# Kernel tuning notes

Hardware: AMD Instinct MI355X
Metric: run time of the kernel (lower is better)

## Reference

```python
import jax, jax.numpy as jnp
import numpy as np

HEADS, DIM_HEAD = 4, 32
EAF_LAMBDA, EAF_ZMAX = 1.0, 4.0
MIN_SIGMA, MAX_SIGMA = 1.0, 8.0

def _gen_grid(h, w):
    xs = np.linspace(0.0, 1.0, w, dtype=np.float32)
    ys = np.linspace(0.0, 1.0, h, dtype=np.float32)
    gy, gx = np.meshgrid(ys, xs, indexing='ij')
    return np.stack([gx, gy, np.ones_like(gx)], 0)  # [3,h,w]

def setup_inputs():
    key = jax.random.key(0)
    ks = jax.random.split(key, 12)
    B, N, C, D = 4, 6, 128, 128
    Hb, Wb, fh, fw = 25, 25, 24, 48
    inner = HEADS * DIM_HEAD
    # BEV ego-plane grid (same math as BEVEmbedding with bev 200x200, 100m, 3 decoder blocks)
    g = _gen_grid(Hb, Wb)
    g[0] *= 200.0
    g[1] *= 200.0
    V = np.array([[0., -2., 100.], [-2., 0., 100.], [0., 0., 1.]], dtype=np.float32)
    bev_grid = (np.linalg.inv(V) @ g.reshape(3, -1)).reshape(3, Hb, Wb)
    # image plane pixel grid (buffer), scaled to 480x224 image
    ip = _gen_grid(fh, fw)[None]
    ip[:, 0] *= 480.0
    ip[:, 1] *= 224.0
    # cam->world extrinsics: 6 surround cameras on a ring
    E_inv = np.zeros((B, N, 4, 4), dtype=np.float32)
    for n in range(N):
        yaw = 2.0 * np.pi * n / N
        c, s = np.cos(yaw), np.sin(yaw)
        E_inv[:, n, :3, :3] = np.array([[c, -s, 0.], [s, c, 0.], [0., 0., 1.]], dtype=np.float32)
        E_inv[:, n, :3, 3] = np.array([2. * c, 2. * s, 1.6], dtype=np.float32)
        E_inv[:, n, 3, 3] = 1.0
    Kmat = np.array([[260., 0., 240.], [0., 260., 112.], [0., 0., 1.]], dtype=np.float32)
    I_inv = np.broadcast_to(np.linalg.inv(Kmat), (B, N, 3, 3)).astype(np.float32).copy()
    w = lambda k, shape: 0.02 * jax.random.normal(k, shape, dtype=jnp.float32)
    return dict(
        x=jax.random.normal(ks[0], (B, D, Hb, Wb), dtype=jnp.float32),
        feature=jax.random.normal(ks[1], (B, N, C, fh, fw), dtype=jnp.float32),
        I_inv=jnp.asarray(I_inv), E_inv=jnp.asarray(E_inv),
        bev_grid=jnp.asarray(bev_grid), image_plane=jnp.asarray(ip),
        bn_v_g=jnp.ones(C), bn_v_b=jnp.zeros(C), bn_v_m=jnp.zeros(C), bn_v_var=jnp.ones(C),
        conv_v_w=w(ks[2], (D, C)),
        bn_k_g=jnp.ones(C), bn_k_b=jnp.zeros(C), bn_k_m=jnp.zeros(C), bn_k_var=jnp.ones(C),
        conv_k_w=w(ks[3], (D, C)),
        ln_q_g=jnp.ones(D), ln_q_b=jnp.zeros(D),
        ln_k_g=jnp.ones(D), ln_k_b=jnp.zeros(D),
        ln_v_g=jnp.ones(D), ln_v_b=jnp.zeros(D),
        Wq=w(ks[4], (inner, D)), bq=jnp.zeros(inner),
        Wk=w(ks[5], (inner, D)), bk=jnp.zeros(inner),
        Wv=w(ks[6], (inner, D)), bv=jnp.zeros(inner),
        Wo=w(ks[7], (D, inner)), bo=jnp.zeros(D),
        ln_pre_g=jnp.ones(D), ln_pre_b=jnp.zeros(D),
        W1=w(ks[8], (2 * D, D)), b1=jnp.zeros(2 * D),
        W2=w(ks[9], (D, 2 * D)), b2=jnp.zeros(D),
        ln_post_g=jnp.ones(D), ln_post_b=jnp.zeros(D),
    )

def _ln(x, g, b):
    m = x.mean(-1, keepdims=True)
    v = ((x - m) ** 2).mean(-1, keepdims=True)
    return (x - m) * jax.lax.rsqrt(v + 1e-5) * g + b

def _bn_relu_conv(f, g, b, mu, var, Wc):
    # inference BatchNorm2d -> ReLU -> 1x1 Conv (no bias)
    f = (f - mu[None, :, None, None]) * (jax.lax.rsqrt(var + 1e-5) * g)[None, :, None, None] + b[None, :, None, None]
    f = jax.nn.relu(f)
    return jnp.einsum('bchw,dc->bdhw', f, Wc)

def reference(x, feature, I_inv, E_inv, bev_grid, image_plane,
              bn_v_g, bn_v_b, bn_v_m, bn_v_var, conv_v_w,
              bn_k_g, bn_k_b, bn_k_m, bn_k_var, conv_k_w,
              ln_q_g, ln_q_b, ln_k_g, ln_k_b, ln_v_g, ln_v_b,
              Wq, bq, Wk, bk, Wv, bv, Wo, bo,
              ln_pre_g, ln_pre_b, W1, b1, W2, b2, ln_post_g, ln_post_b):
    B, N, C, fh, fw = feature.shape
    _, D, Hb, Wb = x.shape
    Q = Hb * Wb
    Kp = fh * fw
    feat = feature.reshape(B * N, C, fh, fw)
    val = _bn_relu_conv(feat, bn_v_g, bn_v_b, bn_v_m, bn_v_var, conv_v_w)
    keyf = _bn_relu_conv(feat, bn_k_g, bn_k_b, bn_k_m, bn_k_var, conv_k_w)
    v = val.reshape(B, N, D, fh, fw)
    k = keyf.reshape(B, N, D, fh, fw)
    # ---- EAF weights ----
    xy = bev_grid[:2].reshape(2, Q).T                      # [Q,2]
    ones = jnp.ones((Q, 1), dtype=bev_grid.dtype)
    P0 = jnp.concatenate([xy, 0.0 * ones, ones], -1)       # [Q,4] z=0
    P1 = jnp.concatenate([xy, EAF_ZMAX * ones, ones], -1)  # [Q,4] z=zmax
    E = jnp.linalg.inv(E_inv)                              # world->cam
    P0c = jnp.einsum('bnij,qj->bnqi', E, P0)
    P1c = jnp.einsum('bnij,qj->bnqi', E, P1)
    Icam = jnp.linalg.inv(I_inv)
    p0 = jnp.einsum('bnij,bnqj->bnqi', Icam, P0c[..., :3])
    p1 = jnp.einsum('bnij,bnqj->bnqi', Icam, P1c[..., :3])
    p0 = p0 / (p0[..., 2:3] + 1e-8)
    p1 = p1 / (p1[..., 2:3] + 1e-8)
    l = jnp.cross(p0, p1)                                  # epipolar line [B,N,Q,3]
    denom = jnp.maximum(jnp.sqrt(l[..., 0] ** 2 + l[..., 1] ** 2), 1e-8)
    l_hat = l / denom[..., None]
    x_img = image_plane[0].reshape(3, Kp).T                # [K,3]
    d = jnp.abs(jnp.einsum('bnqj,kj->bnqk', l_hat, x_img))
    # adaptive lambda_{q,i}
    cam_xy = E_inv[..., :2, 3]                             # [B,N,2]
    vec = xy[None, None] - cam_xy[:, :, None]              # [B,N,Q,2]
    dist = jnp.linalg.norm(vec, axis=-1) + 1e-6
    dist_max = dist.max(axis=(1, 2), keepdims=True) + 1e-6
    dist_norm = jnp.clip(dist / dist_max, 0.0, 1.0)
    sigma = MAX_SIGMA - dist_norm * (MAX_SIGMA - MIN_SIGMA)
    lambda_qi = 1.0 / (sigma + 1e-6)
    scale_w = (EAF_LAMBDA * lambda_qi) ** 2                # [B,N,Q]
    Wmask = jnp.exp(-scale_w[..., None] * d ** 2)          # [B,N,Q,K]
    W_logits = Wmask.transpose(0, 2, 1, 3).reshape(B, Q, N * Kp)
    # ---- cross attention (EAF weight multiplied into logits pre-softmax) ----
    qt = x.reshape(B, D, Q).transpose(0, 2, 1)             # [B,Q,D]
    kt = k.transpose(0, 1, 3, 4, 2).reshape(B, N * Kp, D)
    vt = v.transpose(0, 1, 3, 4, 2).reshape(B, N * Kp, D)
    qp = _ln(qt, ln_q_g, ln_q_b) @ Wq.T + bq
    kp = _ln(kt, ln_k_g, ln_k_b) @ Wk.T + bk
    vp = _ln(vt, ln_v_g, ln_v_b) @ Wv.T + bv
    qh = qp.reshape(B, Q, HEADS, DIM_HEAD).transpose(0, 2, 1, 3)
    kh = kp.reshape(B, N * Kp, HEADS, DIM_HEAD).transpose(0, 2, 1, 3)
    vh = vp.reshape(B, N * Kp, HEADS, DIM_HEAD).transpose(0, 2, 1, 3)
    logits = jnp.einsum('bhqd,bhkd->bhqk', qh, kh) * (DIM_HEAD ** -0.5)
    logits = logits * W_logits[:, None]                    # broadcast over heads
    attn = jax.nn.softmax(logits, axis=-1)
    out = jnp.einsum('bhqk,bhkd->bhqd', attn, vh)
    out = out.transpose(0, 2, 1, 3).reshape(B, Q, HEADS * DIM_HEAD)
    out = out @ Wo.T + bo                                  # [B,Q,D]
    z = out + qt                                           # skip = x
    z = _ln(z, ln_pre_g, ln_pre_b)
    z = z + (jax.nn.gelu(z @ W1.T + b1, approximate=False) @ W2.T + b2)
    z = _ln(z, ln_post_g, ln_post_b)
    return z.transpose(0, 2, 1).reshape(B, D, Hb, Wb)
```

## Files before the change

### kernel.cpp

```cpp
#include <hip/hip_runtime.h>
#include <hip/hip_bf16.h>

typedef unsigned short u16;
typedef __attribute__((ext_vector_type(8))) short short8v;
typedef __attribute__((ext_vector_type(4))) float f32x4;
typedef __attribute__((ext_vector_type(2))) __fp16 fp16x2;

#define B_   4
#define N_   6
#define Q_   625
#define QPAD 640
#define KP_  1152
#define NK_  6912
#define NKB  216
#define NSPLIT 12
#define KSEG (NK_/NSPLIT)
#define FHW  1152
#define LOG2E 1.4426950408889634f
#define LOG2_LOG2E 0.5287663729448977f

__device__ __forceinline__ float bfu(unsigned int u16v){ return __uint_as_float(u16v << 16); }
__device__ __forceinline__ unsigned int f2bfu(float f){
  unsigned int u = __float_as_uint(f);
  return (u + 0x7fffu + ((u>>16)&1u)) >> 16;
}
__device__ __forceinline__ float exp2a(float x){
  float r; asm("v_exp_f32 %0, %1" : "=v"(r) : "v"(x)); return r;
}
__device__ __forceinline__ unsigned cvtpk_bf16(float lo, float hi){
  unsigned r; asm("v_cvt_pk_bf16_f32 %0, %1, %2" : "=v"(r) : "v"(lo), "v"(hi)); return r;
}
__device__ __forceinline__ unsigned cvtpk_f16(float lo, float hi){
  union { fp16x2 h; unsigned u; } c;
  c.h = __builtin_amdgcn_cvt_pkrtz(lo, hi);
  return c.u;
}
__device__ __forceinline__ float ldfeat(const void* p, size_t i, bool isbf){
  return isbf ? bfu((unsigned)reinterpret_cast<const u16*>(p)[i])
              : reinterpret_cast<const float*>(p)[i];
}
union U4S8 { uint4 u; short8v s; };
union H2U { unsigned u; fp16x2 h; };

struct InPack {
  const void* p[38];
  int off[38];
  int sz[38];
  int nseg;
  int total;
};

__global__ __launch_bounds__(256) void k_ingest(InPack P, float* __restrict__ dst,
                                                const unsigned* __restrict__ magic){
  int idx = blockIdx.x*256 + threadIdx.x;
  if (idx >= P.total) return;
  bool isbf = (*magic == 0x3F803F80u);
  int lo=0, hi=P.nseg-1;
  while (lo<hi){ int mid=(lo+hi+1)>>1; if (P.off[mid]<=idx) lo=mid; else hi=mid-1; }
  int j = idx - P.off[lo];
  float v = 0.f;
  if (j < P.sz[lo]){
    v = isbf ? bfu((unsigned)reinterpret_cast<const u16*>(P.p[lo])[j])
             : reinterpret_cast<const float*>(P.p[lo])[j];
  }
  dst[idx] = v;
}

__global__ void k_prep(const float* __restrict__ ckw, const float* __restrict__ cvw,
                       const float* __restrict__ Wk,  const float* __restrict__ Wv,
                       const float* __restrict__ Wq,  const float* __restrict__ Wo,
                       const float* __restrict__ W1,  const float* __restrict__ W2,
                       const float* __restrict__ bkg, const float* __restrict__ bkb,
                       const float* __restrict__ bkm, const float* __restrict__ bkv,
                       const float* __restrict__ bvg, const float* __restrict__ bvb,
                       const float* __restrict__ bvm, const float* __restrict__ bvv,
                       u16* convKbf, u16* convVbf, u16* WkBf, u16* WvBf, u16* WqBf,
                       u16* WoBf, u16* W1Bf, u16* W2Bf,
                       float* csK, float* cbK, float* csV, float* cbV)
{
  int gid = blockIdx.x*256 + threadIdx.x;
  if (gid < 81920){
    int mat = gid >> 14, i = gid & 16383;
    const float* src = mat==0?ckw: mat==1?cvw: mat==2?Wk: mat==3?Wv: Wq;
    u16*         dst = mat==0?convKbf: mat==1?convVbf: mat==2?WkBf: mat==3?WvBf: WqBf;
    dst[i] = (u16)f2bfu(src[i]);
  } else if (gid < 98304){
    int i = gid - 81920; WoBf[i] = (u16)f2bfu(Wo[i]);
  } else if (gid < 131072){
    int i = gid - 98304; W1Bf[i] = (u16)f2bfu(W1[i]);
  } else if (gid < 163840){
    int i = gid - 131072; W2Bf[i] = (u16)f2bfu(W2[i]);
  } else if (gid < 163840+128){
    int c = gid - 163840;
    float s = rsqrtf(bkv[c]+1e-5f)*bkg[c];
    csK[c]=s; cbK[c]=bkb[c] - bkm[c]*s;
  } else if (gid < 163840+256){
    int c = gid - 163840 - 128;
    float s = rsqrtf(bvv[c]+1e-5f)*bvg[c];
    csV[c]=s; cbV[c]=bvb[c] - bvm[c]*s;
  }
}

__global__ void k_distmax(const float* __restrict__ bev, const float* __restrict__ Einv,
                          float* __restrict__ dmax)
{
  int b = blockIdx.x, tid = threadIdx.x;
  float mx = 0.f;
  for (int i = tid; i < N_*Q_; i += 256){
    int n = i / Q_, q = i - n*Q_;
    float x = bev[q], y = bev[Q_+q];
    float cx = Einv[(b*N_+n)*16 + 3], cy = Einv[(b*N_+n)*16 + 7];
    float dx = x-cx, dy = y-cy;
    mx = fmaxf(mx, sqrtf(dx*dx+dy*dy) + 1e-6f);
  }
  __shared__ float red[256];
  red[tid]=mx; __syncthreads();
  for (int s=128;s>0;s>>=1){ if (tid<s) red[tid]=fmaxf(red[tid],red[tid+s]); __syncthreads(); }
  if (tid==0) dmax[b] = red[0] + 1e-6f;
}

__global__ void k_geom(const float* __restrict__ Einv, const float* __restrict__ Iinv,
                       const float* __restrict__ bev, const float* __restrict__ dmax,
                       float* __restrict__ geom)
{
  int idx = blockIdx.x*256 + threadIdx.x;
  if (idx >= B_*N_*Q_) return;
  int b = idx / (N_*Q_), r = idx - b*(N_*Q_), n = r / Q_, q = r - n*Q_;

  float a[4][8];
  #pragma unroll
  for (int i=0;i<4;++i){
    #pragma unroll
    for (int j=0;j<4;++j) a[i][j] = Einv[(b*N_+n)*16 + i*4 + j];
    #pragma unroll
    for (int j=0;j<4;++j) a[i][4+j] = (i==j)?1.f:0.f;
  }
  #pragma unroll
  for (int col=0;col<4;++col){
    float inv = 1.f/a[col][col];
    #pragma unroll
    for (int j=0;j<8;++j) a[col][j]*=inv;
    #pragma unroll
    for (int rr=0;rr<4;++rr) if (rr!=col){
      float f=a[rr][col];
      #pragma unroll
      for (int j=0;j<8;++j) a[rr][j] -= f*a[col][j];
    }
  }
  float E[3][4];
  #pragma unroll
  for (int i=0;i<3;++i)
    #pragma unroll
    for (int j=0;j<4;++j) E[i][j]=a[i][4+j];

  float m9[9];
  #pragma unroll
  for (int i=0;i<9;++i) m9[i] = Iinv[(b*N_+n)*9 + i];
  float c00 =  m9[4]*m9[8]-m9[5]*m9[7];
  float c01 = -(m9[3]*m9[8]-m9[5]*m9[6]);
  float c02 =  m9[3]*m9[7]-m9[4]*m9[6];
  float id = 1.f/(m9[0]*c00 + m9[1]*c01 + m9[2]*c02);
  float Ic[3][3];
  Ic[0][0]=c00*id; Ic[0][1]=-(m9[1]*m9[8]-m9[2]*m9[7])*id; Ic[0][2]=(m9[1]*m9[5]-m9[2]*m9[4])*id;
  Ic[1][0]=c01*id; Ic[1][1]= (m9[0]*m9[8]-m9[2]*m9[6])*id; Ic[1][2]=-(m9[0]*m9[5]-m9[2]*m9[3])*id;
  Ic[2][0]=c02*id; Ic[2][1]=-(m9[0]*m9[7]-m9[1]*m9[6])*id; Ic[2][2]=(m9[0]*m9[4]-m9[1]*m9[3])*id;

  float x = bev[q], y = bev[Q_+q];
  float P0c[3], P1c[3];
  #pragma unroll
  for (int i=0;i<3;++i){
    P0c[i] = E[i][0]*x + E[i][1]*y + E[i][3];
    P1c[i] = E[i][0]*x + E[i][1]*y + E[i][2]*4.0f + E[i][3];
  }
  float p0[3], p1[3];
  #pragma unroll
  for (int i=0;i<3;++i){
    p0[i] = Ic[i][0]*P0c[0] + Ic[i][1]*P0c[1] + Ic[i][2]*P0c[2];
    p1[i] = Ic[i][0]*P1c[0] + Ic[i][1]*P1c[1] + Ic[i][2]*P1c[2];
  }
  float z0 = p0[2]+1e-8f, z1 = p1[2]+1e-8f;
  #pragma unroll
  for (int i=0;i<3;++i){ p0[i]/=z0; p1[i]/=z1; }
  float l0 = p0[1]*p1[2]-p0[2]*p1[1];
  float l1 = p0[2]*p1[0]-p0[0]*p1[2];
  float l2 = p0[0]*p1[1]-p0[1]*p1[0];
  float den = fmaxf(sqrtf(l0*l0+l1*l1), 1e-8f);
  float cx = Einv[(b*N_+n)*16+3], cy = Einv[(b*N_+n)*16+7];
  float dx = x-cx, dy = y-cy;
  float dist = sqrtf(dx*dx+dy*dy) + 1e-6f;
  float dn = fminf(fmaxf(dist/dmax[b], 0.f), 1.f);
  float sigma = 8.0f - dn*7.0f;
  float lam = 1.f/(sigma+1e-6f);
  float* g = geom + (size_t)idx*4;
  g[0]=l0/den; g[1]=l1/den; g[2]=l2/den;
  g[3]=-(lam*lam)*LOG2E;
}

__global__ __launch_bounds__(256) void k_kvproj(
  const void* __restrict__ feat, const unsigned* __restrict__ magic,
  const float* __restrict__ csK, const float* __restrict__ cbK,
  const float* __restrict__ csV, const float* __restrict__ cbV,
  const u16* __restrict__ convKbf, const u16* __restrict__ convVbf,
  const u16* __restrict__ WkBf, const u16* __restrict__ WvBf,
  const float* __restrict__ lkg, const float* __restrict__ lkb,
  const float* __restrict__ lvg, const float* __restrict__ lvb,
  const float* __restrict__ bk_, const float* __restrict__ bv_,
  u16* __restrict__ kp, u16* __restrict__ vpB)
{
  __shared__ __align__(16) unsigned char lds_tile[16384];
  __shared__ float2 redLN[4][64];
  uint4* lds16 = reinterpret_cast<uint4*>(lds_tile);

  const int tid = threadIdx.x;
  const int w = tid >> 6, l = tid & 63;
  const int lr = l & 15, lg4 = l >> 4;
  const int ptile = blockIdx.x;
  const int bn = blockIdx.y, b = bn/6, n = bn - b*6;
  const bool isbf = (*magic == 0x3F803F80u);

  const size_t fbase = (size_t)bn*128*FHW + ptile*64 + l;
  float fv[32];
  #pragma unroll
  for (int pass=0; pass<4; ++pass)
    #pragma unroll
    for (int j=0;j<8;++j){
      int c = pass*32 + w*8 + j;
      fv[pass*8+j] = ldfeat(feat, fbase + (size_t)c*FHW, isbf);
    }

  const int psw = l & 7;
  for (int half=0; half<2; ++half){
    const float* cs   = half ? csV : csK;
    const float* cbv_ = half ? cbV : cbK;
    const u16* convB  = half ? convVbf : convKbf;
    const u16* WB     = half ? WvBf : WkBf;
    const float* lng  = half ? lvg : lkg;
    const float* lnb  = half ? lvb : lkb;
    const float* bias = half ? bv_ : bk_;

    #pragma unroll
    for (int pass=0; pass<4; ++pass){
      int c0 = pass*32 + w*8;
      unsigned int u[4];
      #pragma unroll
      for (int i2=0;i2<4;++i2){
        int ca = c0 + i2*2, cb2 = ca+1;
        float aa = fmaxf(fv[pass*8+i2*2  ]*cs[ca]+cbv_[ca], 0.f);
        float ab = fmaxf(fv[pass*8+i2*2+1]*cs[cb2]+cbv_[cb2], 0.f);
        u[i2] = f2bfu(aa) | (f2bfu(ab)<<16);
      }
      int c8 = c0 >> 3;
      lds16[l*16 + (c8 ^ psw)] = make_uint4(u[0],u[1],u[2],u[3]);
    }
    __syncthreads();

    f32x4 acc[2][4];
    #pragma unroll
    for (int i=0;i<2;++i)
      #pragma unroll
      for (int j=0;j<4;++j) acc[i][j] = (f32x4){0.f,0.f,0.f,0.f};

    #pragma unroll
    for (int ks2=0; ks2<4; ++ks2){
      short8v af[2];
      #pragma unroll
      for (int ib=0; ib<2; ++ib)
        af[ib] = *reinterpret_cast<const short8v*>(convB + ((w*32 + ib*16 + lr)<<7) + (ks2<<5) + (lg4<<3));
      #pragma unroll
      for (int pb2=0; pb2<4; ++pb2){
        int p = pb2*16 + lr;
        U4S8 bu; bu.u = lds16[p*16 + ((ks2*4 + lg4) ^ (p&7))];
        acc[0][pb2] = __builtin_amdgcn_mfma_f32_16x16x32_bf16(af[0], bu.s, acc[0][pb2], 0,0,0);
        acc[1][pb2] = __builtin_amdgcn_mfma_f32_16x16x32_bf16(af[1], bu.s, acc[1][pb2], 0,0,0);
      }
    }

    float s1v[4], s2v[4];
    #pragma unroll
    for (int pb2=0;pb2<4;++pb2){
      float s=0.f, s2=0.f;
      #pragma unroll
      for (int ib=0;ib<2;++ib)
        #pragma unroll
        for (int r=0;r<4;++r){ float v = acc[ib][pb2][r]; s+=v; s2+=v*v; }
      s += __shfl_xor(s,16);  s += __shfl_xor(s,32);
      s2 += __shfl_xor(s2,16); s2 += __shfl_xor(s2,32);
      s1v[pb2]=s; s2v[pb2]=s2;
    }
    if (l < 16){
      #pragma unroll
      for (int pb2=0;pb2<4;++pb2) redLN[w][pb2*16+l] = make_float2(s1v[pb2], s2v[pb2]);
    }
    __syncthreads();

    float mean[4], rstd[4];
    #pragma unroll
    for (int pb2=0;pb2<4;++pb2){
      int p = pb2*16 + lr;
      float2 t0 = redLN[0][p], t1 = redLN[1][p], t2 = redLN[2][p], t3 = redLN[3][p];
      float S = t0.x+t1.x+t2.x+t3.x, S2 = t0.y+t1.y+t2.y+t3.y;
      float mm = S*(1.f/128.f);
      float var = fmaxf(S2*(1.f/128.f) - mm*mm, 0.f);
      mean[pb2] = mm; rstd[pb2] = rsqrtf(var + 1e-5f);
    }
    float4 g4[2], b4[2];
    #pragma unroll
    for (int ib=0;ib<2;++ib){
      g4[ib] = *reinterpret_cast<const float4*>(lng + w*32 + ib*16 + lg4*4);
      b4[ib] = *reinterpret_cast<const float4*>(lnb + w*32 + ib*16 + lg4*4);
    }
    #pragma unroll
    for (int ib=0;ib<2;++ib){
      const float* gg = &g4[ib].x; const float* bb2 = &b4[ib].x;
      int d0 = w*32 + ib*16 + lg4*4;
      int d8 = d0 >> 3, doff = (d0 & 7) * 2;
      #pragma unroll
      for (int pb2=0;pb2<4;++pb2){
        int p = pb2*16 + lr;
        float z0 = (acc[ib][pb2][0]-mean[pb2])*rstd[pb2]*gg[0]+bb2[0];
        float z1 = (acc[ib][pb2][1]-mean[pb2])*rstd[pb2]*gg[1]+bb2[1];
        float z2 = (acc[ib][pb2][2]-mean[pb2])*rstd[pb2]*gg[2]+bb2[2];
        float z3 = (acc[ib][pb2][3]-mean[pb2])*rstd[pb2]*gg[3]+bb2[3];
        unsigned int u0 = f2bfu(z0) | (f2bfu(z1)<<16);
        unsigned int u1 = f2bfu(z2) | (f2bfu(z3)<<16);
        *reinterpret_cast<uint2*>(lds_tile + p*256 + ((d8 ^ (p&7))<<4) + doff) = make_uint2(u0,u1);
      }
    }
    __syncthreads();

    f32x4 acc2[2][4];
    #pragma unroll
    for (int i=0;i<2;++i)
      #pragma unroll
      for (int j=0;j<4;++j) acc2[i][j] = (f32x4){0.f,0.f,0.f,0.f};

    #pragma unroll
    for (int ks2=0; ks2<4; ++ks2){
      short8v af[2];
      #pragma unroll
      for (int ib=0; ib<2; ++ib)
        af[ib] = *reinterpret_cast<const short8v*>(WB + ((w*32 + ib*16 + lr)<<7) + (ks2<<5) + (lg4<<3));
      #pragma unroll
      for (int pb2=0; pb2<4; ++pb2){
        int p = pb2*16 + lr;
        U4S8 bu; bu.u = lds16[p*16 + ((ks2*4 + lg4) ^ (p&7))];
        acc2[0][pb2] = __builtin_amdgcn_mfma_f32_16x16x32_bf16(af[0], bu.s, acc2[0][pb2], 0,0,0);
        acc2[1][pb2] = __builtin_amdgcn_mfma_f32_16x16x32_bf16(af[1], bu.s, acc2[1][pb2], 0,0,0);
      }
    }
    float4 bias4[2];
    #pragma unroll
    for (int ib=0;ib<2;++ib)
      bias4[ib] = *reinterpret_cast<const float4*>(bias + w*32 + ib*16 + lg4*4);

    __syncthreads();

    if (half == 0){
      #pragma unroll
      for (int ib=0;ib<2;++ib){
        const float* bb2 = &bias4[ib].x;
        int i0 = w*32 + ib*16 + lg4*4;
        int i8 = i0 >> 3, ioff = (i0 & 7) * 2;
        #pragma unroll
        for (int pb2=0;pb2<4;++pb2){
          int p = pb2*16 + lr;
          unsigned int u0 = f2bfu(acc2[ib][pb2][0]+bb2[0]) | (f2bfu(acc2[ib][pb2][1]+bb2[1])<<16);
          unsigned int u1 = f2bfu(acc2[ib][pb2][2]+bb2[2]) | (f2bfu(acc2[ib][pb2][3]+bb2[3])<<16);
          *reinterpret_cast<uint2*>(lds_tile + p*256 + ((i8 ^ (p&7))<<4) + ioff) = make_uint2(u0,u1);
        }
      }
      __syncthreads();
      size_t krow0 = (size_t)b*NK_ + n*KP_ + ptile*64;
      #pragma unroll
      for (int kk=0;kk<4;++kk){
        int idx = kk*256 + tid;
        int p = idx >> 4, j = idx & 15;
        uint4 vv = lds16[p*16 + (j ^ (p&7))];
        *reinterpret_cast<uint4*>(kp + (krow0 + p)*128 + j*8) = vv;
      }
    } else {
      u16* lds2 = reinterpret_cast<u16*>(lds_tile);
      #pragma unroll
      for (int ib=0;ib<2;++ib){
        const float* bb2 = &bias4[ib].x;
        int i0 = w*32 + ib*16 + lg4*4;
        #pragma unroll
        for (int pb2=0;pb2<4;++pb2){
          int p = pb2*16 + lr;
          int pc = ((p&12)<<1) | (p&3) | ((p&16)>>2) | (p&32);
          #pragma unroll
          for (int r=0;r<4;++r)
            lds2[(i0+r)*64 + pc] = (u16)f2bfu(acc2[ib][pb2][r]+bb2[r]);
        }
      }
      __syncthreads();
      int kb0 = b*NKB + n*(KP_/32) + ptile*2;
      #pragma unroll
      for (int kk=0;kk<4;++kk){
        int idx = kk*256 + tid;
        int p2 = idx >> 9, d = (idx>>2)&127, ch = idx&3;
        uint4 vv = lds16[d*8 + p2*4 + ch];
        *reinterpret_cast<uint4*>(vpB + ((size_t)(kb0+p2)*128 + d)*32 + ch*8) = vv;
      }
    }
    __syncthreads();
  }
}

__global__ __launch_bounds__(256) void k_qprojM(
  const float* __restrict__ x, const float* __restrict__ lg, const float* __restrict__ lb,
  const u16* __restrict__ WqBf, const float* __restrict__ bq_, u16* __restrict__ qp)
{
  const float SCL = 0.17677669529663687f;
  __shared__ __align__(16) unsigned char lds_tile[16384];
  __shared__ float redS[4][64], redS2[4][64];
  uint4* lds16 = reinterpret_cast<uint4*>(lds_tile);

  const int tid = threadIdx.x;
  const int w = tid >> 6, l = tid & 63;
  const int lr = l & 15, lg4 = l >> 4;
  const int q0 = blockIdx.x * 64;
  const int b  = blockIdx.y;

  int qg = q0 + l; if (qg > Q_-1) qg = Q_-1;
  float xv[32];
  float s = 0.f, s2 = 0.f;
  #pragma unroll
  for (int i=0;i<32;++i){
    float v = x[(size_t)(b*128 + w*32 + i)*Q_ + qg];
    xv[i] = v; s += v; s2 += v*v;
  }
  redS[w][l] = s; redS2[w][l] = s2;
  __syncthreads();
  float S  = redS[0][l]+redS[1][l]+redS[2][l]+redS[3][l];
  float S2 = redS2[0][l]+redS2[1][l]+redS2[2][l]+redS2[3][l];
  float mm = S*(1.f/128.f);
  float rs = rsqrtf(fmaxf(S2*(1.f/128.f)-mm*mm, 0.f) + 1e-5f);
  #pragma unroll
  for (int j=0;j<4;++j){
    unsigned u[4];
    #pragma unroll
    for (int c2=0;c2<4;++c2){
      int i = j*8 + c2*2;
      int d = w*32 + i;
      float z0 = (xv[i]  -mm)*rs*lg[d]   + lb[d];
      float z1 = (xv[i+1]-mm)*rs*lg[d+1] + lb[d+1];
      u[c2] = f2bfu(z0) | (f2bfu(z1)<<16);
    }
    int d8 = w*4 + j;
    lds16[l*16 + (d8 ^ (l&7))] = make_uint4(u[0],u[1],u[2],u[3]);
  }
  __syncthreads();

  f32x4 acc2[2][4];
  #pragma unroll
  for (int i=0;i<2;++i)
    #pragma unroll
    for (int j=0;j<4;++j) acc2[i][j] = (f32x4){0.f,0.f,0.f,0.f};

  #pragma unroll
  for (int ks2=0; ks2<4; ++ks2){
    short8v af[2];
    #pragma unroll
    for (int ib=0; ib<2; ++ib)
      af[ib] = *reinterpret_cast<const short8v*>(WqBf + ((w*32 + ib*16 + lr)<<7) + (ks2<<5) + (lg4<<3));
    #pragma unroll
    for (int pb2=0; pb2<4; ++pb2){
      int p = pb2*16 + lr;
      U4S8 bu; bu.u = lds16[p*16 + ((ks2*4 + lg4) ^ (p&7))];
      acc2[0][pb2] = __builtin_amdgcn_mfma_f32_16x16x32_bf16(af[0], bu.s, acc2[0][pb2], 0,0,0);
      acc2[1][pb2] = __builtin_amdgcn_mfma_f32_16x16x32_bf16(af[1], bu.s, acc2[1][pb2], 0,0,0);
    }
  }
  float4 bias4[2];
  #pragma unroll
  for (int ib=0;ib<2;++ib)
    bias4[ib] = *reinterpret_cast<const float4*>(bq_ + w*32 + ib*16 + lg4*4);

  __syncthreads();
  #pragma unroll
  for (int ib=0;ib<2;++ib){
    const float* bb2 = &bias4[ib].x;
    int i0 = w*32 + ib*16 + lg4*4;
    int i8 = i0 >> 3, ioff = (i0 & 7) * 2;
    #pragma unroll
    for (int pb2=0;pb2<4;++pb2){
      int p = pb2*16 + lr;
      unsigned int u0 = f2bfu((acc2[ib][pb2][0]+bb2[0])*SCL) | (f2bfu((acc2[ib][pb2][1]+bb2[1])*SCL)<<16);
      unsigned int u1 = f2bfu((acc2[ib][pb2][2]+bb2[2])*SCL) | (f2bfu((acc2[ib][pb2][3]+bb2[3])*SCL)<<16);
      *reinterpret_cast<uint2*>(lds_tile + p*256 + ((i8 ^ (p&7))<<4) + ioff) = make_uint2(u0,u1);
    }
  }
  __syncthreads();
  #pragma unroll
  for (int kk=0;kk<4;++kk){
    int idx = kk*256 + tid;
    int p = idx >> 4, j = idx & 15;
    uint4 vv = lds16[p*16 + (j ^ (p&7))];
    *reinterpret_cast<uint4*>(qp + (size_t)(b*QPAD + q0 + p)*128 + j*8) = vv;
  }
}

__global__ __launch_bounds__(256) void k_attn(
    const u16* __restrict__ qp, const u16* __restrict__ kp, const u16* __restrict__ vpB,
    const float* __restrict__ geom, const float* __restrict__ ip,
    float* __restrict__ part)
{
  __shared__ uint4 ldsK[2][512];
  __shared__ u16  ldsW[2][32*36];

  const int tid = threadIdx.x;
  const int h = tid >> 6;
  const int lane = tid & 63;
  const int lq = lane & 15;
  const int g  = lane >> 4;
  const int bid = blockIdx.x;
  const int b = bid / (20*NSPLIT);
  const int r = bid - b*(20*NSPLIT);
  const int qt = r / NSPLIT;
  const int ks = r - qt*NSPLIT;
  const int q0 = qt*32;
  const int qa = q0 + lq;
  const int qb = q0 + 16 + lq;

  short8v bq0 = *reinterpret_cast<const short8v*>(qp + ((size_t)(b*QPAD + qa))*128 + h*32 + g*8);
  short8v bq1 = *reinterpret_cast<const short8v*>(qp + ((size_t)(b*QPAD + qb))*128 + h*32 + g*8);

  f32x4 o00={0,0,0,0}, o01={0,0,0,0}, o10={0,0,0,0}, o11={0,0,0,0};
  f32x4 zero4 = {0.f,0.f,0.f,0.f};
  float psum0 = 0.f, psum1 = 0.f;

  const int kbeg = ks*KSEG, kend = kbeg + KSEG;
  const int n0 = kbeg / KP_;
  const int pb0 = kbeg - n0*KP_;

  const int wq = tid >> 3, wc = tid & 7;
  int qwg = q0 + wq; if (qwg > Q_-1) qwg = Q_-1;
  const float* gw_ = geom + ((size_t)((b*N_+n0)*Q_ + qwg))*4;
  const float wl0 = gw_[0], wl1 = gw_[1], wl2 = gw_[2], wgw = gw_[3];

  const int c2 = tid*2;
  const int kr0 = c2 >> 4, kch = c2 & 15;
  auto STAGE = [&](int buf, int k0){
    const uint4* gk = reinterpret_cast<const uint4*>(kp + (size_t)(b*NK_ + k0)*128);
    uint4 k0v = gk[c2], k1v = gk[c2+1];
    ldsK[buf][kr0*16 + (kch     ^ (kr0&7))] = k0v;
    ldsK[buf][kr0*16 + ((kch+1) ^ (kr0&7))] = k1v;
  };
  auto WSTAGE = [&](int buf, int k0){
    int key = pb0 + (k0 - kbeg) + wc*4;
    float4 xx = *reinterpret_cast<const float4*>(ip + key);
    float4 yy = *reinterpret_cast<const float4*>(ip + KP_ + key);
    const float* xp = &xx.x; const float* yp = &yy.x;
    float wv[4];
    #pragma unroll
    for (int i=0;i<4;++i){
      float dln = fmaf(wl0, xp[i], fmaf(wl1, yp[i], wl2));
      wv[i] = exp2a(fmaf(wgw, dln*dln, LOG2_LOG2E));
    }
    uint2 pk;
    pk.x = cvtpk_f16(wv[0], wv[1]);
    pk.y = cvtpk_f16(wv[2], wv[3]);
    *reinterpret_cast<uint2*>(&ldsW[buf][wq*36 + wc*4]) = pk;
  };

  const uint4* vpb4 = reinterpret_cast<const uint4*>(vpB);
  const int dd = h*32 + lq;
  const int iv0 = dd*4 + g, iv1 = (dd+16)*4 + g;
  auto VPAN = [&](int k0){ return vpb4 + ((size_t)(b*NKB + (k0>>5)))*512; };

  STAGE(0, kbeg);
  WSTAGE(0, kbeg);
  U4S8 vc0, vc1;
  { const uint4* vp = VPAN(kbeg); vc0.u = vp[iv0]; vc1.u = vp[iv1]; }

  int cur = 0;
  const int kchunk = h*4 + g;
  for (int k0 = kbeg; k0 < kend; k0 += 32){
    __syncthreads();
    bool more = (k0 + 32) < kend;
    if (more){ STAGE(cur^1, k0+32); WSTAGE(cur^1, k0+32); }
    int kn = more ? (k0 + 32) : k0;
    U4S8 vn0, vn1;
    { const uint4* vp = VPAN(kn); vn0.u = vp[iv0]; vn1.u = vp[iv1]; }

    uint2 wA0 = *reinterpret_cast<const uint2*>(&ldsW[cur][lq*36 + g*4]);
    uint2 wA1 = *reinterpret_cast<const uint2*>(&ldsW[cur][lq*36 + 16 + g*4]);
    uint2 wB0 = *reinterpret_cast<const uint2*>(&ldsW[cur][(16+lq)*36 + g*4]);
    uint2 wB1 = *reinterpret_cast<const uint2*>(&ldsW[cur][(16+lq)*36 + 16 + g*4]);
    float w00[4], w01[4], w10[4], w11[4];
    {
      H2U t0,t1,t2,t3,t4,t5,t6,t7;
      t0.u=wA0.x; t1.u=wA0.y; t2.u=wA1.x; t3.u=wA1.y;
      t4.u=wB0.x; t5.u=wB0.y; t6.u=wB1.x; t7.u=wB1.y;
      w00[0]=(float)t0.h[0]; w00[1]=(float)t0.h[1]; w00[2]=(float)t1.h[0]; w00[3]=(float)t1.h[1];
      w01[0]=(float)t2.h[0]; w01[1]=(float)t2.h[1]; w01[2]=(float)t3.h[0]; w01[3]=(float)t3.h[1];
      w10[0]=(float)t4.h[0]; w10[1]=(float)t4.h[1]; w10[2]=(float)t5.h[0]; w10[3]=(float)t5.h[1];
      w11[0]=(float)t6.h[0]; w11[1]=(float)t6.h[1]; w11[2]=(float)t7.h[0]; w11[3]=(float)t7.h[1];
    }

    __builtin_amdgcn_s_setprio(1);
    U4S8 a0, a1;
    a0.u = ldsK[cur][lq*16      + (kchunk ^ (lq&7))];
    a1.u = ldsK[cur][(16+lq)*16 + (kchunk ^ (lq&7))];
    f32x4 s00 = __builtin_amdgcn_mfma_f32_16x16x32_bf16(a0.s, bq0, zero4, 0,0,0);
    f32x4 s01 = __builtin_amdgcn_mfma_f32_16x16x32_bf16(a1.s, bq0, zero4, 0,0,0);
    f32x4 s10 = __builtin_amdgcn_mfma_f32_16x16x32_bf16(a0.s, bq1, zero4, 0,0,0);
    f32x4 s11 = __builtin_amdgcn_mfma_f32_16x16x32_bf16(a1.s, bq1, zero4, 0,0,0);

    float p00[4], p01[4], p10[4], p11[4];
    #pragma unroll
    for (int r2=0;r2<4;++r2){
      p00[r2] = exp2a(fmaf(s00[r2], w00[r2], -8.f));
      p01[r2] = exp2a(fmaf(s01[r2], w01[r2], -8.f));
      psum0 += p00[r2] + p01[r2];
      p10[r2] = exp2a(fmaf(s10[r2], w10[r2], -8.f));
      p11[r2] = exp2a(fmaf(s11[r2], w11[r2], -8.f));
      psum1 += p10[r2] + p11[r2];
    }
    union { short8v s; unsigned int u[4]; } bp0, bp1;
    bp0.u[0] = cvtpk_bf16(p00[0], p00[1]);
    bp0.u[1] = cvtpk_bf16(p00[2], p00[3]);
    bp0.u[2] = cvtpk_bf16(p01[0], p01[1]);
    bp0.u[3] = cvtpk_bf16(p01[2], p01[3]);
    bp1.u[0] = cvtpk_bf16(p10[0], p10[1]);
    bp1.u[1] = cvtpk_bf16(p10[2], p10[3]);
    bp1.u[2] = cvtpk_bf16(p11[0], p11[1]);
    bp1.u[3] = cvtpk_bf16(p11[2], p11[3]);

    o00 = __builtin_amdgcn_mfma_f32_16x16x32_bf16(vc0.s, bp0.s, o00, 0,0,0);
    o01 = __builtin_amdgcn_mfma_f32_16x16x32_bf16(vc1.s, bp0.s, o01, 0,0,0);
    o10 = __builtin_amdgcn_mfma_f32_16x16x32_bf16(vc0.s, bp1.s, o10, 0,0,0);
    o11 = __builtin_amdgcn_mfma_f32_16x16x32_bf16(vc1.s, bp1.s, o11, 0,0,0);
    __builtin_amdgcn_s_setprio(0);

    vc0 = vn0; vc1 = vn1;
    cur ^= 1;
  }
  psum0 += __shfl_xor(psum0,16);
  psum0 += __shfl_xor(psum0,32);
  psum1 += __shfl_xor(psum1,16);
  psum1 += __shfl_xor(psum1,32);
  int slot0 = ((b*4 + h)*40 + qt*2    )*NSPLIT + ks;
  int slot1 = ((b*4 + h)*40 + qt*2 + 1)*NSPLIT + ks;
  float* pr0 = part + ((size_t)slot0*16 + lq)*34;
  float* pr1 = part + ((size_t)slot1*16 + lq)*34;
  #pragma unroll
  for (int r2=0;r2<4;++r2){
    pr0[g*4+r2] = o00[r2]; pr0[16+g*4+r2] = o01[r2];
    pr1[g*4+r2] = o10[r2]; pr1[16+g*4+r2] = o11[r2];
  }
  if (g==0){ pr0[33] = psum0; pr1[33] = psum1; }
}

__global__ __launch_bounds__(256) void k_epiM(
  const float* __restrict__ part, const float* __restrict__ x,
  const u16* __restrict__ WoBf, const float* __restrict__ bo_,
  const float* __restrict__ lpg, const float* __restrict__ lpb,
  const u16* __restrict__ W1Bf, const float* __restrict__ b1_,
  const u16* __restrict__ W2Bf, const float* __restrict__ b2_,
  const float* __restrict__ lsg, const float* __restrict__ lsb,
  void* __restrict__ out, const unsigned* __restrict__ magic)
{
  const float ISQ2 = 0.7071067811865476f;
  __shared__ __align__(16) unsigned char lds_tile[16384];
  __shared__ __align__(16) unsigned char lds_h1[32768];
  __shared__ float2 redLN[4][64];
  uint4* lds16 = reinterpret_cast<uint4*>(lds_tile);
  uint4* ldsH  = reinterpret_cast<uint4*>(lds_h1);

  const int tid = threadIdx.x;
  const int w = tid >> 6, l = tid & 63;
  const int lr = l & 15, lg4 = l >> 4;
  const int q0 = blockIdx.x * 64;
  const int b  = blockIdx.y;
  const bool isbf = (*magic == 0x3F803F80u);

  {
    int qg = q0 + l; if (qg > Q_-1) qg = Q_-1;
    int qt = qg >> 4, qq = qg & 15;
    const float* base = part + (size_t)(((b*4+w)*40+qt)*NSPLIT)*544 + qq*34;
    float den = 0.f;
    #pragma unroll
    for (int s=0;s<NSPLIT;++s) den += base[s*544 + 33];
    float rden = 1.f/den;
    float num[32];
    #pragma unroll
    for (int i=0;i<32;++i) num[i]=0.f;
    #pragma unroll
    for (int s=0;s<NSPLIT;++s){
      const float* bp = base + s*544;
      #pragma unroll
      for (int i=0;i<32;++i) num[i] += bp[i];
    }
    #pragma unroll
    for (int j=0;j<4;++j){
      unsigned u[4];
      #pragma unroll
      for (int c2=0;c2<4;++c2){
        int i = j*8 + c2*2;
        u[c2] = f2bfu(num[i]*rden) | (f2bfu(num[i+1]*rden)<<16);
      }
      int d8 = w*4 + j;
      lds16[l*16 + (d8 ^ (l&7))] = make_uint4(u[0],u[1],u[2],u[3]);
    }
  }
  __syncthreads();

  f32x4 acc[2][4];
  #pragma unroll
  for (int i=0;i<2;++i)
    #pragma unroll
    for (int j=0;j<4;++j) acc[i][j] = (f32x4){0.f,0.f,0.f,0.f};
  #pragma unroll
  for (int ks2=0; ks2<4; ++ks2){
    short8v af[2];
    #pragma unroll
    for (int ib=0; ib<2; ++ib)
      af[ib] = *reinterpret_cast<const short8v*>(WoBf + ((w*32 + ib*16 + lr)<<7) + (ks2<<5) + (lg4<<3));
    #pragma unroll
    for (int pb2=0; pb2<4; ++pb2){
      int p = pb2*16 + lr;
      U4S8 bu; bu.u = lds16[p*16 + ((ks2*4 + lg4) ^ (p&7))];
      acc[0][pb2] = __builtin_amdgcn_mfma_f32_16x16x32_bf16(af[0], bu.s, acc[0][pb2], 0,0,0);
      acc[1][pb2] = __builtin_amdgcn_mfma_f32_16x16x32_bf16(af[1], bu.s, acc[1][pb2], 0,0,0);
    }
  }
  float4 bo4[2];
  #pragma unroll
  for (int ib=0;ib<2;++ib)
    bo4[ib] = *reinterpret_cast<const float4*>(bo_ + w*32 + ib*16 + lg4*4);
  f32x4 zv[2][4];
  #pragma unroll
  for (int ib=0;ib<2;++ib){
    const float* bb2 = &bo4[ib].x;
    #pragma unroll
    for (int pb2=0;pb2<4;++pb2){
      int qq2 = q0 + pb2*16 + lr; if (qq2 > Q_-1) qq2 = Q_-1;
      #pragma unroll
      for (int r=0;r<4;++r){
        int i = w*32 + ib*16 + lg4*4 + r;
        zv[ib][pb2][r] = acc[ib][pb2][r] + bb2[r] + x[(size_t)(b*128 + i)*Q_ + qq2];
      }
    }
  }
  float s1v[4], s2v[4];
  #pragma unroll
  for (int pb2=0;pb2<4;++pb2){
    float s=0.f, s2=0.f;
    #pragma unroll
    for (int ib=0;ib<2;++ib)
      #pragma unroll
      for (int r=0;r<4;++r){ float v = zv[ib][pb2][r]; s+=v; s2+=v*v; }
    s += __shfl_xor(s,16);  s += __shfl_xor(s,32);
    s2 += __shfl_xor(s2,16); s2 += __shfl_xor(s2,32);
    s1v[pb2]=s; s2v[pb2]=s2;
  }
  if (l < 16){
    #pragma unroll
    for (int pb2=0;pb2<4;++pb2) redLN[w][pb2*16+l] = make_float2(s1v[pb2], s2v[pb2]);
  }
  __syncthreads();
  float mean1[4], rstd1[4];
  #pragma unroll
  for (int pb2=0;pb2<4;++pb2){
    int p = pb2*16 + lr;
    float2 t0 = redLN[0][p], t1 = redLN[1][p], t2 = redLN[2][p], t3 = redLN[3][p];
    float S = t0.x+t1.x+t2.x+t3.x, S2 = t0.y+t1.y+t2.y+t3.y;
    float mm = S*(1.f/128.f);
    float var = fmaxf(S2*(1.f/128.f) - mm*mm, 0.f);
    mean1[pb2] = mm; rstd1[pb2] = rsqrtf(var + 1e-5f);
  }
  float4 lg4v[2], lb4v[2];
  #pragma unroll
  for (int ib=0;ib<2;++ib){
    lg4v[ib] = *reinterpret_cast<const float4*>(lpg + w*32 + ib*16 + lg4*4);
    lb4v[ib] = *reinterpret_cast<const float4*>(lpb + w*32 + ib*16 + lg4*4);
  }
  #pragma unroll
  for (int ib=0;ib<2;++ib){
    const float* gg = &lg4v[ib].x; const float* bb2 = &lb4v[ib].x;
    int d0 = w*32 + ib*16 + lg4*4;
    int d8 = d0 >> 3, doff = (d0 & 7) * 2;
    #pragma unroll
    for (int pb2=0;pb2<4;++pb2){
      int p = pb2*16 + lr;
      #pragma unroll
      for (int r=0;r<4;++r)
        zv[ib][pb2][r] = (zv[ib][pb2][r]-mean1[pb2])*rstd1[pb2]*gg[r]+bb2[r];
      unsigned int u0 = f2bfu(zv[ib][pb2][0]) | (f2bfu(zv[ib][pb2][1])<<16);
      unsigned int u1 = f2bfu(zv[ib][pb2][2]) | (f2bfu(zv[ib][pb2][3])<<16);
      *reinterpret_cast<uint2*>(lds_tile + p*256 + ((d8 ^ (p&7))<<4) + doff) = make_uint2(u0,u1);
    }
  }
  __syncthreads();

  f32x4 acc1[4][4];
  #pragma unroll
  for (int i=0;i<4;++i)
    #pragma unroll
    for (int j=0;j<4;++j) acc1[i][j] = (f32x4){0.f,0.f,0.f,0.f};
  #pragma unroll
  for (int ks2=0; ks2<4; ++ks2){
    short8v af[4];
    #pragma unroll
    for (int fi=0; fi<4; ++fi)
      af[fi] = *reinterpret_cast<const short8v*>(W1Bf + ((w*64 + fi*16 + lr)<<7) + (ks2<<5) + (lg4<<3));
    #pragma unroll
    for (int pb2=0; pb2<4; ++pb2){
      int p = pb2*16 + lr;
      U4S8 bu; bu.u = lds16[p*16 + ((ks2*4 + lg4) ^ (p&7))];
      #pragma unroll
      for (int fi=0; fi<4; ++fi)
        acc1[fi][pb2] = __builtin_amdgcn_mfma_f32_16x16x32_bf16(af[fi], bu.s, acc1[fi][pb2], 0,0,0);
    }
  }
  #pragma unroll
  for (int fi=0; fi<4; ++fi){
    float4 b14 = *reinterpret_cast<const float4*>(b1_ + w*64 + fi*16 + lg4*4);
    const float* bb2 = &b14.x;
    int i10 = w*64 + fi*16 + lg4*4;
    int ch = i10 >> 3, ioff = (i10 & 7) * 2;
    #pragma unroll
    for (int pb2=0;pb2<4;++pb2){
      int p = pb2*16 + lr;
      float gl[4];
      #pragma unroll
      for (int r=0;r<4;++r){
        float hh = acc1[fi][pb2][r] + bb2[r];
        gl[r] = 0.5f*hh*(1.f+erff(hh*ISQ2));
      }
      unsigned int u0 = f2bfu(gl[0]) | (f2bfu(gl[1])<<16);
      unsigned int u1 = f2bfu(gl[2]) | (f2bfu(gl[3])<<16);
      *reinterpret_cast<uint2*>(lds_h1 + p*512 + ((ch ^ (p&7))<<4) + ioff) = make_uint2(u0,u1);
    }
  }
  __syncthreads();

  f32x4 acc2[2][4];
  #pragma unroll
  for (int i=0;i<2;++i)
    #pragma unroll
    for (int j=0;j<4;++j) acc2[i][j] = (f32x4){0.f,0.f,0.f,0.f};
  #pragma unroll
  for (int ks2=0; ks2<8; ++ks2){
    short8v af[2];
    #pragma unroll
    for (int ib=0; ib<2; ++ib)
      af[ib] = *reinterpret_cast<const short8v*>(W2Bf + (w*32 + ib*16 + lr)*256 + ks2*32 + lg4*8);
    #pragma unroll
    for (int pb2=0; pb2<4; ++pb2){
      int p = pb2*16 + lr;
      U4S8 bu; bu.u = ldsH[p*32 + ((ks2*4 + lg4) ^ (p&7))];
      acc2[0][pb2] = __builtin_amdgcn_mfma_f32_16x16x32_bf16(af[0], bu.s, acc2[0][pb2], 0,0,0);
      acc2[1][pb2] = __builtin_amdgcn_mfma_f32_16x16x32_bf16(af[1], bu.s, acc2[1][pb2], 0,0,0);
    }
  }
  float4 b24[2];
  #pragma unroll
  for (int ib=0;ib<2;++ib)
    b24[ib] = *reinterpret_cast<const float4*>(b2_ + w*32 + ib*16 + lg4*4);
  f32x4 z2[2][4];
  #pragma unroll
  for (int ib=0;ib<2;++ib){
    const float* bb2 = &b24[ib].x;
    #pragma unroll
    for (int pb2=0;pb2<4;++pb2)
      #pragma unroll
      for (int r=0;r<4;++r)
        z2[ib][pb2][r] = zv[ib][pb2][r] + acc2[ib][pb2][r] + bb2[r];
  }
  #pragma unroll
  for (int pb2=0;pb2<4;++pb2){
    float s=0.f, s2=0.f;
    #pragma unroll
    for (int ib=0;ib<2;++ib)
      #pragma unroll
      for (int r=0;r<4;++r){ float v = z2[ib][pb2][r]; s+=v; s2+=v*v; }
    s += __shfl_xor(s,16);  s += __shfl_xor(s,32);
    s2 += __shfl_xor(s2,16); s2 += __shfl_xor(s2,32);
    s1v[pb2]=s; s2v[pb2]=s2;
  }
  __syncthreads();
  if (l < 16){
    #pragma unroll
    for (int pb2=0;pb2<4;++pb2) redLN[w][pb2*16+l] = make_float2(s1v[pb2], s2v[pb2]);
  }
  __syncthreads();
  float4 sg4[2], sb4[2];
  #pragma unroll
  for (int ib=0;ib<2;++ib){
    sg4[ib] = *reinterpret_cast<const float4*>(lsg + w*32 + ib*16 + lg4*4);
    sb4[ib] = *reinterpret_cast<const float4*>(lsb + w*32 + ib*16 + lg4*4);
  }
  #pragma unroll
  for (int pb2=0;pb2<4;++pb2){
    int p = pb2*16 + lr;
    int q = q0 + p;
    if (q >= Q_) continue;
    float2 t0 = redLN[0][p], t1 = redLN[1][p], t2 = redLN[2][p], t3 = redLN[3][p];
    float S = t0.x+t1.x+t2.x+t3.x, S2 = t0.y+t1.y+t2.y+t3.y;
    float mm = S*(1.f/128.f);
    float rs = rsqrtf(fmaxf(S2*(1.f/128.f) - mm*mm, 0.f) + 1e-5f);
    #pragma unroll
    for (int ib=0;ib<2;++ib){
      const float* gg = &sg4[ib].x; const float* bb2 = &sb4[ib].x;
      #pragma unroll
      for (int r=0;r<4;++r){
        int i = w*32 + ib*16 + lg4*4 + r;
        float z3 = (z2[ib][pb2][r]-mm)*rs*gg[r] + bb2[r];
        size_t oidx = (size_t)(b*128+i)*Q_ + q;
        if (isbf) reinterpret_cast<u16*>(out)[oidx] = (u16)f2bfu(z3);
        else      reinterpret_cast<float*>(out)[oidx] = z3;
      }
    }
  }
}

extern "C" void kernel_launch(void* const* d_in, const int* in_sizes, int n_in,
                              void* d_out, int out_size, void* d_ws, size_t ws_size,
                              hipStream_t stream){
  InPack P;
  int nseg = n_in < 38 ? n_in : 38;
  int c = 0;
  for (int i=0;i<nseg;++i){
    P.p[i] = d_in[i];
    P.off[i] = c;
    P.sz[i] = (i == 1) ? 0 : in_sizes[i];
    c += (P.sz[i] + 7) & ~7;
  }
  P.nseg = nseg;
  P.total = c;

  float* fw = (float*)d_ws;
  float* fin = fw;
  const float* fx    = fin + P.off[0];
  const float* fIinv = fin + P.off[2];
  const float* fEinv = fin + P.off[3];
  const float* fbev  = fin + P.off[4];
  const float* fip   = fin + P.off[5];
  const float* fbvg  = fin + P.off[6];
  const float* fbvb  = fin + P.off[7];
  const float* fbvm  = fin + P.off[8];
  const float* fbvv  = fin + P.off[9];
  const float* fcvw  = fin + P.off[10];
  const float* fbkg  = fin + P.off[11];
  const float* fbkb  = fin + P.off[12];
  const float* fbkm  = fin + P.off[13];
  const float* fbkv  = fin + P.off[14];
  const float* fckw  = fin + P.off[15];
  const float* flqg  = fin + P.off[16];
  const float* flqb  = fin + P.off[17];
  const float* flkg  = fin + P.off[18];
  const float* flkb  = fin + P.off[19];
  const float* flvg  = fin + P.off[20];
  const float* flvb  = fin + P.off[21];
  const float* fWq   = fin + P.off[22];
  const float* fbq   = fin + P.off[23];
  const float* fWk   = fin + P.off[24];
  const float* fbk   = fin + P.off[25];
  const float* fWv   = fin + P.off[26];
  const float* fbv   = fin + P.off[27];
  const float* fWo   = fin + P.off[28];
  const float* fbo   = fin + P.off[29];
  const float* flpg  = fin + P.off[30];
  const float* flpb  = fin + P.off[31];
  const float* fW1   = fin + P.off[32];
  const float* fb1   = fin + P.off[33];
  const float* fW2   = fin + P.off[34];
  const float* fb2   = fin + P.off[35];
  const float* flsg  = fin + P.off[36];
  const float* flsb  = fin + P.off[37];

  size_t off = (size_t)P.total;
  float* geomW = fin + off;  off += 60000;
  float* dmaxW = fin + off;  off += 8;
  float* csK = fin + off;    off += 128;
  float* cbK = fin + off;    off += 128;
  float* csV = fin + off;    off += 128;
  float* cbV = fin + off;    off += 128;
  float* part = fin + off;   off += (size_t)B_*4*40*NSPLIT*544;
  u16* bb = (u16*)(fin + off);
  u16* convKbf = bb;
  u16* convVbf = bb + 16384;
  u16* WkBf    = bb + 32768;
  u16* WvBf    = bb + 49152;
  u16* WqBf    = bb + 65536;
  u16* WoBf    = bb + 81920;
  u16* W1Bf    = bb + 98304;
  u16* W2Bf    = bb + 131072;
  u16* kp  = bb + 163840;
  u16* vpB = kp + (size_t)B_*NK_*128;
  u16* qp  = vpB + (size_t)B_*NK_*128;

  const unsigned* magic = (const unsigned*)d_in[6];
  const void* featRaw = d_in[1];

  k_ingest<<<(P.total+255)/256,256,0,stream>>>(P, fin, magic);
  k_prep<<<641,256,0,stream>>>(fckw,fcvw,fWk,fWv,fWq,fWo,fW1,fW2,
                               fbkg,fbkb,fbkm,fbkv, fbvg,fbvb,fbvm,fbvv,
                               convKbf,convVbf,WkBf,WvBf,WqBf,WoBf,W1Bf,W2Bf,
                               csK,cbK,csV,cbV);
  k_distmax<<<4,256,0,stream>>>(fbev, fEinv, dmaxW);
  k_geom<<<59,256,0,stream>>>(fEinv, fIinv, fbev, dmaxW, geomW);
  k_kvproj<<<dim3(18,24),256,0,stream>>>(featRaw, magic, csK,cbK,csV,cbV, convKbf,convVbf,
                                         WkBf,WvBf, flkg,flkb,flvg,flvb, fbk,fbv, kp, vpB);
  k_qprojM<<<dim3(10,B_),256,0,stream>>>(fx, flqg,flqb, WqBf, fbq, qp);
  k_attn<<<B_*20*NSPLIT,256,0,stream>>>(qp, kp, vpB, geomW, fip, part);
  k_epiM<<<dim3(10,B_),256,0,stream>>>(part, fx, WoBf,fbo, flpg,flpb, W1Bf,fb1, W2Bf,fb2,
                                       flsg,flsb, d_out, magic);
}
```

Measured before the change: 103.3 us.

## Double attention key splits and fold weight prep into ingest kernel

Raises the number of key-dimension splits in the attention kernel from 12 to 24, which doubles the grid and shortens each split's sequential work. The epilogue reduction loops are only partially unrolled to cope with the longer split count. Separately, the weight bf16 conversion and batch-norm folding are merged into the ingest kernel, reading directly from the raw inputs, which removes one kernel launch and its dependency. More splits mean more partial-result traffic and more reduction work in the epilogue.

Result: slower. 114.6 us (+10.9%).

```diff
diff --git a/kernel.cpp b/kernel.cpp
--- a/kernel.cpp
+++ b/kernel.cpp
@@ -13,7 +13,7 @@
 #define KP_  1152
 #define NK_  6912
 #define NKB  216
-#define NSPLIT 12
+#define NSPLIT 24
 #define KSEG (NK_/NSPLIT)
 #define FHW  1152
 #define LOG2E 1.4426950408889634f
@@ -51,53 +51,44 @@
 };
 
 __global__ __launch_bounds__(256) void k_ingest(InPack P, float* __restrict__ dst,
-                                                const unsigned* __restrict__ magic){
+                                                const unsigned* __restrict__ magic,
+                                                u16* __restrict__ wbf,
+                                                float* __restrict__ csK, float* __restrict__ cbK,
+                                                float* __restrict__ csV, float* __restrict__ cbV){
   int idx = blockIdx.x*256 + threadIdx.x;
-  if (idx >= P.total) return;
   bool isbf = (*magic == 0x3F803F80u);
-  int lo=0, hi=P.nseg-1;
-  while (lo<hi){ int mid=(lo+hi+1)>>1; if (P.off[mid]<=idx) lo=mid; else hi=mid-1; }
-  int j = idx - P.off[lo];
-  float v = 0.f;
-  if (j < P.sz[lo]){
-    v = isbf ? bfu((unsigned)reinterpret_cast<const u16*>(P.p[lo])[j])
-             : reinterpret_cast<const float*>(P.p[lo])[j];
-  }
-  dst[idx] = v;
-}
-
-__global__ void k_prep(const float* __restrict__ ckw, const float* __restrict__ cvw,
-                       const float* __restrict__ Wk,  const float* __restrict__ Wv,
-                       const float* __restrict__ Wq,  const float* __restrict__ Wo,
-                       const float* __restrict__ W1,  const float* __restrict__ W2,
-                       const float* __restrict__ bkg, const float* __restrict__ bkb,
-                       const float* __restrict__ bkm, const float* __restrict__ bkv,
-                       const float* __restrict__ bvg, const float* __restrict__ bvb,
-                       const float* __restrict__ bvm, const float* __restrict__ bvv,
-                       u16* convKbf, u16* convVbf, u16* WkBf, u16* WvBf, u16* WqBf,
-                       u16* WoBf, u16* W1Bf, u16* W2Bf,
-                       float* csK, float* cbK, float* csV, float* cbV)
-{
-  int gid = blockIdx.x*256 + threadIdx.x;
-  if (gid < 81920){
-    int mat = gid >> 14, i = gid & 16383;
-    const float* src = mat==0?ckw: mat==1?cvw: mat==2?Wk: mat==3?Wv: Wq;
-    u16*         dst = mat==0?convKbf: mat==1?convVbf: mat==2?WkBf: mat==3?WvBf: WqBf;
-    dst[i] = (u16)f2bfu(src[i]);
-  } else if (gid < 98304){
-    int i = gid - 81920; WoBf[i] = (u16)f2bfu(Wo[i]);
-  } else if (gid < 131072){
-    int i = gid - 98304; W1Bf[i] = (u16)f2bfu(W1[i]);
-  } else if (gid < 163840){
-    int i = gid - 131072; W2Bf[i] = (u16)f2bfu(W2[i]);
-  } else if (gid < 163840+128){
-    int c = gid - 163840;
-    float s = rsqrtf(bkv[c]+1e-5f)*bkg[c];
-    csK[c]=s; cbK[c]=bkb[c] - bkm[c]*s;
-  } else if (gid < 163840+256){
-    int c = gid - 163840 - 128;
-    float s = rsqrtf(bvv[c]+1e-5f)*bvg[c];
-    csV[c]=s; cbV[c]=bvb[c] - bvm[c]*s;
+  if (idx < P.total){
+    int lo=0, hi=P.nseg-1;
+    while (lo<hi){ int mid=(lo+hi+1)>>1; if (P.off[mid]<=idx) lo=mid; else hi=mid-1; }
+    int j = idx - P.off[lo];
+    float v = 0.f;
+    if (j < P.sz[lo]) v = ldfeat(P.p[lo], j, isbf);
+    dst[idx] = v;
+    return;
+  }
+  int e = idx - P.total;
+  if (e < 81920){
+    int mat = e >> 14, i = e & 16383;
+    int srcIdx = mat==0?15: mat==1?10: mat==2?24: mat==3?26: 22;
+    wbf[e] = (u16)f2bfu(ldfeat(P.p[srcIdx], i, isbf));
+  } else if (e < 98304){
+    wbf[e] = (u16)f2bfu(ldfeat(P.p[28], e-81920, isbf));
+  } else if (e < 131072){
+    wbf[e] = (u16)f2bfu(ldfeat(P.p[32], e-98304, isbf));
+  } else if (e < 163840){
+    wbf[e] = (u16)f2bfu(ldfeat(P.p[34], e-131072, isbf));
+  } else if (e < 163840+128){
+    int c = e - 163840;
+    float g = ldfeat(P.p[11], c, isbf), bb = ldfeat(P.p[12], c, isbf);
+    float m = ldfeat(P.p[13], c, isbf), vv = ldfeat(P.p[14], c, isbf);
+    float s = rsqrtf(vv+1e-5f)*g;
+    csK[c]=s; cbK[c]=bb - m*s;
+  } else if (e < 163840+256){
+    int c = e - 163840 - 128;
+    float g = ldfeat(P.p[6], c, isbf), bb = ldfeat(P.p[7], c, isbf);
+    float m = ldfeat(P.p[8], c, isbf), vv = ldfeat(P.p[9], c, isbf);
+    float s = rsqrtf(vv+1e-5f)*g;
+    csV[c]=s; cbV[c]=bb - m*s;
   }
 }
 
@@ -681,13 +672,13 @@
     int qt = qg >> 4, qq = qg & 15;
     const float* base = part + (size_t)(((b*4+w)*40+qt)*NSPLIT)*544 + qq*34;
     float den = 0.f;
-    #pragma unroll
+    #pragma unroll 4
     for (int s=0;s<NSPLIT;++s) den += base[s*544 + 33];
     float rden = 1.f/den;
     float num[32];
     #pragma unroll
     for (int i=0;i<32;++i) num[i]=0.f;
-    #pragma unroll
+    #pragma unroll 4
     for (int s=0;s<NSPLIT;++s){
       const float* bp = base + s*544;
       #pragma unroll
@@ -939,35 +930,19 @@
   const float* fEinv = fin + P.off[3];
   const float* fbev  = fin + P.off[4];
   const float* fip   = fin + P.off[5];
-  const float* fbvg  = fin + P.off[6];
-  const float* fbvb  = fin + P.off[7];
-  const float* fbvm  = fin + P.off[8];
-  const float* fbvv  = fin + P.off[9];
-  const float* fcvw  = fin + P.off[10];
-  const float* fbkg  = fin + P.off[11];
-  const float* fbkb  = fin + P.off[12];
-  const float* fbkm  = fin + P.off[13];
-  const float* fbkv  = fin + P.off[14];
-  const float* fckw  = fin + P.off[15];
-  const float* flqg  = fin + P.off[16];
-  const float* flqb  = fin + P.off[17];
   const float* flkg  = fin + P.off[18];
   const float* flkb  = fin + P.off[19];
   const float* flvg  = fin + P.off[20];
   const float* flvb  = fin + P.off[21];
-  const float* fWq   = fin + P.off[22];
+  const float* flqg  = fin + P.off[16];
+  const float* flqb  = fin + P.off[17];
   const float* fbq   = fin + P.off[23];
-  const float* fWk   = fin + P.off[24];
   const float* fbk   = fin + P.off[25];
-  const float* fWv   = fin + P.off[26];
   const float* fbv   = fin + P.off[27];
-  const float* fWo   = fin + P.off[28];
   const float* fbo   = fin + P.off[29];
   const float* flpg  = fin + P.off[30];
   const float* flpb  = fin + P.off[31];
-  const float* fW1   = fin + P.off[32];
   const float* fb1   = fin + P.off[33];
-  const float* fW2   = fin + P.off[34];
   const float* fb2   = fin + P.off[35];
   const float* flsg  = fin + P.off[36];
   const float* flsb  = fin + P.off[37];
@@ -996,11 +971,8 @@
   const unsigned* magic = (const unsigned*)d_in[6];
   const void* featRaw = d_in[1];
 
-  k_ingest<<<(P.total+255)/256,256,0,stream>>>(P, fin, magic);
-  k_prep<<<641,256,0,stream>>>(fckw,fcvw,fWk,fWv,fWq,fWo,fW1,fW2,
-                               fbkg,fbkb,fbkm,fbkv, fbvg,fbvb,fbvm,fbvv,
-                               convKbf,convVbf,WkBf,WvBf,WqBf,WoBf,W1Bf,W2Bf,
-                               csK,cbK,csV,cbV);
+  int ingestTot = P.total + 163840 + 256;
+  k_ingest<<<(ingestTot+255)/256,256,0,stream>>>(P, fin, magic, bb, csK,cbK,csV,cbV);
   k_distmax<<<4,256,0,stream>>>(fbev, fEinv, dmaxW);
   k_geom<<<59,256,0,stream>>>(fEinv, fIinv, fbev, dmaxW, geomW);
   k_kvproj<<<dim3(18,24),256,0,stream>>>(featRaw, magic, csK,cbK,csV,cbV, convKbf,convVbf,
```
